# Performance work log

Measured on AMD Instinct MI355X. Metric: run time of the kernel, lower is better.

The kernel has to match this reference:

```python
import jax, jax.numpy as jnp
import numpy as np

EPS = 1e-5

def splice(x, offsets):
    # x: [B, F, T]; offsets already shifted so offsets[0] == 0.
    # Output channel order matches torch reshape(-1, C*F): y[b, f*C+c, t] = x[b, f, t+off[c]]
    w = offsets[-1]
    Tn = x.shape[2] - w
    y = jnp.stack([x[:, :, o:o + Tn] for o in offsets], axis=2)  # [B, F, C, Tn]
    B, F, C, _ = y.shape
    return y.reshape(B, F * C, Tn)

def conv1x1(x, w, b):
    # x: [B, Cin, T], w: [Cout, Cin], b: [Cout]
    return jnp.einsum('oc,bct->bot', w, x) + b[None, :, None]

def bn_ct(x, gamma=None, beta=None):
    # BatchNorm1d (training mode, biased var) over (batch, time) per channel
    m = x.mean(axis=(0, 2), keepdims=True)
    v = x.var(axis=(0, 2), keepdims=True)
    y = (x - m) * jax.lax.rsqrt(v + EPS)
    if gamma is not None:
        y = y * gamma[None, :, None] + beta[None, :, None]
    return y

def bn_c(x, gamma, beta):
    # BatchNorm1d on [B, C]
    m = x.mean(axis=0, keepdims=True)
    v = x.var(axis=0, keepdims=True)
    return (x - m) * jax.lax.rsqrt(v + EPS) * gamma[None, :] + beta[None, :]

def relu6(x):
    return jnp.clip(x, 0.0, 6.0)

def setup_inputs() -> dict:
    key = jax.random.key(0)
    ks = list(jax.random.split(key, 32))
    def rn(shape, scale=0.05):
        return jax.random.normal(ks.pop(), shape, dtype=jnp.float32) * scale
    inp = {
        'x': jax.random.normal(ks.pop(), (32, 2048, 20), dtype=jnp.float32),
        'h1_w': rn((512, 100)), 'h1_b': rn((512,)),
        'h2_w': rn((512, 1536)), 'h2_b': rn((512,)),
        'bn2_g': jnp.ones((512,), jnp.float32), 'bn2_b': jnp.zeros((512,), jnp.float32),
        'h3_w': rn((512, 1536)), 'h3_b': rn((512,)),
        'bn3_g': jnp.ones((512,), jnp.float32), 'bn3_b': jnp.zeros((512,), jnp.float32),
        'h4_w': rn((512, 512)), 'h4_b': rn((512,)),
        'bn4_g': jnp.ones((512,), jnp.float32), 'bn4_b': jnp.zeros((512,), jnp.float32),
        'h5_w': rn((1500, 512)), 'h5_b': rn((1500,)),
        'bn5_g': jnp.ones((1500,), jnp.float32), 'bn5_b': jnp.zeros((1500,), jnp.float32),
        'l1_w': rn((512, 3000)), 'l1_b': rn((512,)),
        'bn6_g': jnp.ones((512,), jnp.float32), 'bn6_b': jnp.zeros((512,), jnp.float32),
        'l2_w': rn((512, 512)), 'l2_b': rn((512,)),
        'bn7_g': jnp.ones((512,), jnp.float32), 'bn7_b': jnp.zeros((512,), jnp.float32),
    }
    return inp

def reference(x, h1_w, h1_b, h2_w, h2_b, bn2_g, bn2_b, h3_w, h3_b, bn3_g, bn3_b,
              h4_w, h4_b, bn4_g, bn4_b, h5_w, h5_b, bn5_g, bn5_b,
              l1_w, l1_b, bn6_g, bn6_b, l2_w, l2_b, bn7_g, bn7_b):
    o = jnp.transpose(x, (0, 2, 1))                     # [B, 20, T]
    o = splice(o, (0, 1, 2, 3, 4))                      # context [-2..2] -> [B, 100, T-4]
    o = bn_ct(jax.nn.relu(conv1x1(o, h1_w, h1_b)))      # bn1 affine=False
    o = splice(o, (0, 2, 4))                            # context [-2,0,2] -> [B, 1536, T-8]
    o = bn_ct(jax.nn.relu(conv1x1(o, h2_w, h2_b)), bn2_g, bn2_b)
    o = splice(o, (0, 3, 6))                            # context [-3,0,3] -> [B, 1536, T-14]
    o = bn_ct(jax.nn.relu(conv1x1(o, h3_w, h3_b)), bn3_g, bn3_b)
    o = bn_ct(relu6(conv1x1(o, h4_w, h4_b)), bn4_g, bn4_b)
    o = bn_ct(relu6(conv1x1(o, h5_w, h5_b)), bn5_g, bn5_b)  # [B, 1500, T']
    mean = o.mean(axis=-1)
    std = jnp.std(o, axis=-1, ddof=1)                   # torch.std is unbiased
    o = jnp.concatenate((mean, std), axis=1)            # [B, 3000]
    o = bn_c(relu6(o @ l1_w.T + l1_b), bn6_g, bn6_b)
    o = bn_c(relu6(o @ l2_w.T + l2_b), bn7_g, bn7_b)
    return o
```

## Files before the change

### kernel.cpp

```cpp
#include <hip/hip_runtime.h>
#include <cstdint>

#define EPSF 1e-5f

namespace {

typedef _Float16 f16;
typedef _Float16 v8h __attribute__((ext_vector_type(8)));
typedef float v4f __attribute__((ext_vector_type(4)));

constexpr int B  = 32;
constexpr int T0 = 2048, F0 = 20;
constexpr int T1 = 2044, T2 = 2040, T3 = 2034;
constexpr int TS = 2048;

__device__ __forceinline__ void gload16(const void* g, void* l) {
    typedef const __attribute__((address_space(1))) void* gp_t;
    typedef __attribute__((address_space(3))) void* lp_t;
    __builtin_amdgcn_global_load_lds((gp_t)(unsigned long long)g,
                                     (lp_t)(unsigned int)(unsigned long long)l,
                                     16, 0, 0);
}
__device__ __forceinline__ void wait_vm6() { asm volatile("s_waitcnt vmcnt(6)" ::: "memory"); }
__device__ __forceinline__ void wait_vm4() { asm volatile("s_waitcnt vmcnt(4)" ::: "memory"); }
__device__ __forceinline__ void wait_vm0() { asm volatile("s_waitcnt vmcnt(0)" ::: "memory"); }

#define BARRIER asm volatile("s_barrier" ::: "memory")

__global__ __launch_bounds__(256) void transpose_x(const float* __restrict__ x,
                                                   f16* __restrict__ xT,
                                                   float* __restrict__ stZ)
{
    int idx = blockIdx.x * 256 + threadIdx.x;
    if (idx < 4096) stZ[idx] = 0.f;
    constexpr int total = B * 3 * TS * 8;
    if (idx >= total) return;
    int fl = idx & 7;
    int t  = (idx >> 3) & (TS - 1);
    int fo = (idx >> 14) % 3;
    int b  = idx / (3 << 14);
    int f  = fo * 8 + fl;
    float v = (f < F0) ? x[((size_t)b * T0 + t) * F0 + f] : 0.f;
    xT[idx] = (f16)v;
}

template<int FP, int C>
__global__ __launch_bounds__(256) void fold_mfma(
    const float* __restrict__ W, const float* __restrict__ bias,
    const float* __restrict__ st, const float* __restrict__ gamma, const float* __restrict__ beta,
    f16* __restrict__ Wh, float* __restrict__ bf,
    int Oreal, int Freal, int Cin, int CinOrig, float invN)
{
    int o = blockIdx.x;
    auto sidx = [&](int k) {
        return ((size_t)((o >> 7) * (Cin >> 3) + (k >> 3)) * 128 + (o & 127)) * 8 + (k & 7);
    };
    if (o >= Oreal) {
        for (int k = threadIdx.x; k < Cin; k += 256) Wh[sidx(k)] = (f16)0.f;
        if (threadIdx.x == 0) bf[o] = 0.f;
        return;
    }
    float local = 0.f;
    for (int k = threadIdx.x; k < Cin; k += 256) {
        int c = k / FP, f = k - c * FP;
        float wv = 0.f;
        if (c < C && f < Freal) {
            float sc = 1.f, sh = 0.f;
            if (st) {
                float mean = st[f] * invN;
                float var  = st[Freal + f] * invN - mean * mean;
                sc = rsqrtf(var + EPSF);
                if (gamma) sc *= gamma[f];
                sh = (beta ? beta[f] : 0.f) - mean * sc;
            }
            float w = W[(size_t)o * CinOrig + f * C + c];
            wv = w * sc;
            local += w * sh;
        }
        Wh[sidx(k)] = (f16)wv;
    }
#pragma unroll
    for (int d = 32; d; d >>= 1) local += __shfl_down(local, d);
    __shared__ float red[4];
    if ((threadIdx.x & 63) == 0) red[threadIdx.x >> 6] = local;
    __syncthreads();
    if (threadIdx.x == 0) bf[o] = bias[o] + red[0] + red[1] + red[2] + red[3];
}

template<int ACT, int FPR, int CIN>
__global__ __launch_bounds__(256, 4) void conv_mfma(
    const f16* __restrict__ inT, const f16* __restrict__ Wh,
    const float* __restrict__ bias, f16* __restrict__ outT,
    float* __restrict__ st, int O, int Tout, int offMul)
{
    __shared__ __align__(16) f16 Ilds[2][4 * 128 * 8];
    __shared__ __align__(16) f16 Wlds[2][4 * 128 * 8];
    __shared__ float redS[2][128];
    __shared__ float redQ[2][128];
    const int tid  = threadIdx.x;
    const int lane = tid & 63, wave = tid >> 6;
    const int wt = wave & 1, wo = wave >> 1;
    const int quad = lane >> 4, l16 = lane & 15;
    const int tB = blockIdx.x * 128, oB = blockIdx.y * 128, b = blockIdx.z;
    const f16* inb = inT + (size_t)b * FPR * TS;
    const size_t wBase = (size_t)(oB >> 7) * (CIN >> 3);

    v4f acc[4][4];
#pragma unroll
    for (int mi = 0; mi < 4; ++mi)
#pragma unroll
        for (int ni = 0; ni < 4; ++ni)
#pragma unroll
            for (int r = 0; r < 4; ++r) acc[mi][ni][r] = 0.f;

    constexpr int nIter = CIN >> 5;

    auto compute = [&](int pb) {
        v8h afr[4], bfr[4];
#pragma unroll
        for (int mi = 0; mi < 4; ++mi)
            afr[mi] = *(const v8h*)&Ilds[pb][(quad * 128 + wt * 64 + mi * 16 + l16) * 8];
#pragma unroll
        for (int ni = 0; ni < 4; ++ni)
            bfr[ni] = *(const v8h*)&Wlds[pb][(quad * 128 + wo * 64 + ni * 16 + l16) * 8];
#pragma unroll
        for (int mi = 0; mi < 4; ++mi)
#pragma unroll
            for (int ni = 0; ni < 4; ++ni)
                acc[mi][ni] = __builtin_amdgcn_mfma_f32_16x16x32_f16(
                    afr[mi], bfr[ni], acc[mi][ni], 0, 0, 0);
    };

    auto stage = [&](int iB, int pb) {
#pragma unroll
        for (int j = 0; j < 4; ++j) {
            int s = wave * 4 + j;
            int koct = (s & 7) >> 1, half = s & 1;
            if (s < 8) {
                int kidx = iB + koct * 8;
                int c = kidx / FPR, f = kidx - c * FPR;
                int t = tB + half * 64 + lane + c * offMul;
                gload16(inb + ((size_t)(f >> 3) * TS + t) * 8,
                        &Ilds[pb][(koct * 128 + half * 64) * 8]);
            } else {
                gload16(Wh + ((wBase + (iB >> 3) + koct) * 128 + half * 64 + lane) * 8,
                        &Wlds[pb][(koct * 128 + half * 64) * 8]);
            }
        }
    };
    stage(0, 0);
#pragma unroll 2
    for (int k = 0; k < nIter; ++k) {
        const int pb = k & 1;
        __syncthreads();
        if (k + 1 < nIter) { stage((k + 1) * 32, pb ^ 1); wait_vm4(); }
        else               { wait_vm0(); }
        __syncthreads();
        compute(pb);
    }

    float Sl[4] = {0, 0, 0, 0}, Ql[4] = {0, 0, 0, 0};
#pragma unroll
    for (int ni = 0; ni < 4; ++ni) {
        const int o  = oB + wo * 64 + ni * 16 + l16;
        const float bs = bias[o];
        f16* orow = outT + (size_t)b * O * TS + (size_t)(o >> 3) * TS * 8 + (o & 7);
#pragma unroll
        for (int mi = 0; mi < 4; ++mi)
#pragma unroll
            for (int r = 0; r < 4; ++r) {
                int t = tB + wt * 64 + mi * 16 + quad * 4 + r;
                if (t < Tout) {
                    float v = acc[mi][ni][r] + bs;
                    v = fmaxf(v, 0.f);
                    if (ACT == 2) v = fminf(v, 6.f);
                    orow[(size_t)t * 8] = (f16)v;
                    Sl[ni] += v; Ql[ni] += v * v;
                }
            }
    }
#pragma unroll
    for (int ni = 0; ni < 4; ++ni) {
        float s = Sl[ni], q = Ql[ni];
        s += __shfl_down(s, 32); q += __shfl_down(q, 32);
        s += __shfl_down(s, 16); q += __shfl_down(q, 16);
        if (lane < 16) {
            redS[wt][wo * 64 + ni * 16 + lane] = s;
            redQ[wt][wo * 64 + ni * 16 + lane] = q;
        }
    }
    __syncthreads();
    if (tid < 128) {
        atomicAdd(&st[oB + tid],       redS[0][tid] + redS[1][tid]);
        atomicAdd(&st[512 + oB + tid], redQ[0][tid] + redQ[1][tid]);
    }
}


#define LDSB_M(PB, NH) do {                                                          \
    _Pragma("unroll")                                                                \
    for (int n2 = 0; n2 < 2; ++n2) {                                                 \
        _Pragma("unroll")                                                            \
        for (int ks = 0; ks < 2; ++ks)                                               \
            bfr[NH][n2][ks] = *(const v8h*)&Wlds[PB][((ks * 4 + quad) * 256 +        \
                (NH) * 128 + wo * 32 + n2 * 16 + l16) * 8];                          \
    }                                                                                \
} while (0)

#define MFMA_Q(MH, NH) do {                                                          \
    asm volatile("s_waitcnt lgkmcnt(0)" ::: "memory");                               \
    __builtin_amdgcn_sched_barrier(0);                                               \
    __builtin_amdgcn_s_setprio(1);                                                   \
    _Pragma("unroll")                                                                \
    for (int m4 = 0; m4 < 4; ++m4) {                                                 \
        _Pragma("unroll")                                                            \
        for (int n2 = 0; n2 < 2; ++n2) {                                             \
            _Pragma("unroll")                                                        \
            for (int ks = 0; ks < 2; ++ks)                                           \
                acc[(MH) * 4 + m4][(NH) * 2 + n2] =                                  \
                    __builtin_amdgcn_mfma_f32_16x16x32_f16(                          \
                        afr[m4][ks], bfr[NH][n2][ks],                                \
                        acc[(MH) * 4 + m4][(NH) * 2 + n2], 0, 0, 0);                 \
        }                                                                            \
    }                                                                                \
    __builtin_amdgcn_s_setprio(0);                                                   \
} while (0)

template<int ACT, int CIN, bool POOL>
__global__ __launch_bounds__(512, 2) void conv8p(
    const f16* __restrict__ inT, const f16* __restrict__ Wh,
    const float* __restrict__ bias, f16* __restrict__ outT,
    float* __restrict__ st, float* __restrict__ Sp, float* __restrict__ Qp,
    int O, int Tout, int offMul, int Opad)
{
    constexpr bool SPLICE = (CIN == 1536);
    constexpr int NT = CIN / 64;
    constexpr int nIter = NT / 2;
    __shared__ __align__(16) f16 Ilds[2][8 * 256 * 8];
    __shared__ __align__(16) f16 Wlds[2][8 * 256 * 8];
    __shared__ float redS[8][64];
    __shared__ float redQ[8][64];

    const int tid = threadIdx.x;
    const int lane = tid & 63, wave = tid >> 6;
    const int wt = wave & 1, wo = wave >> 1;
    const int quad = lane >> 4, l16 = lane & 15;
    const int tB = blockIdx.x * 256, oB = blockIdx.y * 256, b = blockIdx.z;
    const f16* inb = inT + (size_t)b * 64 * TS * 8;
    const int sBase = oB >> 7;
    const int octSel = tid >> 7;
    const int tPos = tid & 127;

    auto stageA = [&](int pb, int kt, int mh) {
#pragma unroll
        for (int cc = 0; cc < 2; ++cc) {
            const int octL = cc * 4 + octSel;
            const int octG = kt * 8 + octL;
            const int t = tB + mh * 128 + tPos;
            const f16* src;
            if constexpr (SPLICE) {
                const int cx = octG >> 6;
                const int fo = octG & 63;
                src = inb + ((size_t)fo * TS + t + cx * offMul) * 8;
            } else {
                src = inb + ((size_t)octG * TS + t) * 8;
            }
            gload16(src, &Ilds[pb][(octL * 256 + mh * 128 + tPos) * 8]);
        }
    };
    auto stageB = [&](int pb, int kt, int nh) {
#pragma unroll
        for (int cc = 0; cc < 2; ++cc) {
            const int octL = cc * 4 + octSel;
            const f16* src = Wh + (((size_t)(sBase + nh) * (CIN >> 3) + kt * 8 + octL) * 128 + tPos) * 8;
            gload16(src, &Wlds[pb][(octL * 256 + nh * 128 + tPos) * 8]);
        }
    };

    v4f acc[8][4];
#pragma unroll
    for (int m = 0; m < 8; ++m)
#pragma unroll
        for (int n = 0; n < 4; ++n)
#pragma unroll
            for (int r = 0; r < 4; ++r) acc[m][n][r] = 0.f;

    v8h afr[4][2];
    v8h bfr[2][2][2];

    auto ldsA = [&](int pb, int mh) {
#pragma unroll
        for (int m4 = 0; m4 < 4; ++m4)
#pragma unroll
            for (int ks = 0; ks < 2; ++ks)
                afr[m4][ks] = *(const v8h*)&Ilds[pb][((ks * 4 + quad) * 256 +
                    mh * 128 + wt * 64 + m4 * 16 + l16) * 8];
    };

    stageA(0, 0, 0); stageB(0, 0, 0);
    stageB(0, 0, 1); stageA(0, 0, 1);
    stageA(1, 1, 0); stageB(1, 1, 0); stageB(1, 1, 1);
    wait_vm6();
    BARRIER;

#pragma unroll 1
    for (int i = 0; i < nIter; ++i) {
        const int kt1 = 2 * i + 1;
        const int kn0 = 2 * i + 2, kn1 = 2 * i + 3;
        const bool more = (i + 1 < nIter);
        ldsA(0, 0); LDSB_M(0, 0);
        stageA(1, kt1, 1);
        BARRIER;
        MFMA_Q(0, 0);
        BARRIER;
        LDSB_M(0, 1);
        if (more) stageA(0, kn0, 0);
        BARRIER;
        MFMA_Q(0, 1);
        BARRIER;
        ldsA(0, 1);
        if (more) stageB(0, kn0, 0);
        BARRIER;
        MFMA_Q(1, 0);
        BARRIER;
        if (more) { stageB(0, kn0, 1); wait_vm6(); } else wait_vm0();
        BARRIER;
        MFMA_Q(1, 1);
        BARRIER;
        ldsA(1, 0); LDSB_M(1, 0);
        if (more) stageA(0, kn0, 1);
        BARRIER;
        MFMA_Q(0, 0);
        BARRIER;
        LDSB_M(1, 1);
        if (more) stageA(1, kn1, 0);
        BARRIER;
        MFMA_Q(0, 1);
        BARRIER;
        ldsA(1, 1);
        if (more) stageB(1, kn1, 0);
        BARRIER;
        MFMA_Q(1, 0);
        BARRIER;
        if (more) { stageB(1, kn1, 1); wait_vm6(); }
        BARRIER;
        MFMA_Q(1, 1);
        BARRIER;
    }

    float Sl[4] = {0, 0, 0, 0}, Ql[4] = {0, 0, 0, 0};
#pragma unroll
    for (int n = 0; n < 4; ++n) {
        const int oLoc = (n >> 1) * 128 + wo * 32 + (n & 1) * 16 + l16;
        const int o = oB + oLoc;
        const float bs = bias[o];
        f16* orow = nullptr;
        if constexpr (!POOL)
            orow = outT + (size_t)b * O * TS + (size_t)(o >> 3) * TS * 8 + (o & 7);
#pragma unroll
        for (int m = 0; m < 8; ++m)
#pragma unroll
            for (int r = 0; r < 4; ++r) {
                const int t = tB + (m >> 2) * 128 + wt * 64 + (m & 3) * 16 + quad * 4 + r;
                if (t < Tout) {
                    float v = acc[m][n][r] + bs;
                    v = fmaxf(v, 0.f);
                    if (ACT == 2) v = fminf(v, 6.f);
                    if constexpr (!POOL) orow[(size_t)t * 8] = (f16)v;
                    Sl[n] += v; Ql[n] += v * v;
                }
            }
    }
#pragma unroll
    for (int n = 0; n < 4; ++n) {
        float s = Sl[n], q = Ql[n];
        s += __shfl_down(s, 32); q += __shfl_down(q, 32);
        s += __shfl_down(s, 16); q += __shfl_down(q, 16);
        if (lane < 16) { redS[wave][n * 16 + lane] = s; redQ[wave][n * 16 + lane] = q; }
    }
    __syncthreads();
    if (tid < 256) {
        const int rem = tid & 127;
        const int wo2 = rem >> 5;
        const int nn  = (tid >> 7) * 2 + ((rem >> 4) & 1);
        const int l   = tid & 15;
        const float s = redS[wo2 * 2][nn * 16 + l] + redS[wo2 * 2 + 1][nn * 16 + l];
        const float q = redQ[wo2 * 2][nn * 16 + l] + redQ[wo2 * 2 + 1][nn * 16 + l];
        if constexpr (POOL) {
            Sp[((size_t)blockIdx.x * B + b) * Opad + oB + tid] = s;
            Qp[((size_t)blockIdx.x * B + b) * Opad + oB + tid] = q;
        } else {
            atomicAdd(&st[oB + tid], s);
            atomicAdd(&st[512 + oB + tid], q);
        }
    }
}

__global__ __launch_bounds__(256) void pool_finalize(
    const float* __restrict__ Sp, const float* __restrict__ Qp,
    const float* __restrict__ g5, const float* __restrict__ b5,
    float* __restrict__ stat, int Opad, int Oreal, int T)
{
    int co = blockIdx.x * 256 + threadIdx.x;
    if (co >= Oreal) return;
    double sS = 0, sQ = 0;
    for (int z = 0; z < 8; ++z)
        for (int b = 0; b < B; ++b) {
            sS += Sp[((size_t)z * B + b) * Opad + co];
            sQ += Qp[((size_t)z * B + b) * Opad + co];
        }
    double invN = 1.0 / ((double)B * T);
    double m = sS * invN;
    double v = sQ * invN - m * m;
    float sc = g5[co] * rsqrtf((float)v + EPSF);
    float sh = b5[co] - (float)m * sc;
    for (int b = 0; b < B; ++b) {
        double sb = 0, qb = 0;
        for (int z = 0; z < 8; ++z) {
            sb += Sp[((size_t)z * B + b) * Opad + co];
            qb += Qp[((size_t)z * B + b) * Opad + co];
        }
        double mb = sb / T;
        double vb = (qb - sb * sb / T) / (T - 1);
        if (vb < 0) vb = 0;
        stat[(size_t)b * 2 * Oreal + co]         = (float)mb * sc + sh;
        stat[(size_t)b * 2 * Oreal + Oreal + co] = sqrtf((float)vb) * fabsf(sc);
    }
}

__global__ __launch_bounds__(256) void fc_relu6(const float* __restrict__ x,
                                                const float* __restrict__ W,
                                                const float* __restrict__ bias,
                                                float* __restrict__ y, int Cin, int O)
{
    int wid = (blockIdx.x * 256 + threadIdx.x) >> 6;
    int lane = threadIdx.x & 63;
    if (wid >= B * O) return;
    int b = wid / O, o = wid - b * O;
    const float* xr = x + (size_t)b * Cin;
    const float* wr = W + (size_t)o * Cin;
    float s = 0.f;
    for (int c = lane; c < Cin; c += 64) s = fmaf(xr[c], wr[c], s);
#pragma unroll
    for (int d = 32; d; d >>= 1) s += __shfl_down(s, d);
    if (lane == 0) y[wid] = fminf(fmaxf(s + bias[o], 0.f), 6.f);
}

__global__ __launch_bounds__(512) void bn_batch(const float* __restrict__ x,
                                                const float* __restrict__ g,
                                                const float* __restrict__ be,
                                                float* __restrict__ y, int O)
{
    int o = threadIdx.x;
    if (o >= O) return;
    float s = 0.f, q = 0.f;
    for (int b = 0; b < B; ++b) { float v = x[b * O + o]; s += v; q += v * v; }
    float m = s / B;
    float var = q / B - m * m;
    float sc = g[o] * rsqrtf(var + EPSF);
    float sh = be[o] - m * sc;
    for (int b = 0; b < B; ++b) y[b * O + o] = x[b * O + o] * sc + sh;
}

}

extern "C" void kernel_launch(void* const* d_in, const int* in_sizes, int n_in,
                              void* d_out, int out_size, void* d_ws, size_t ws_size,
                              hipStream_t stream)
{
    (void)in_sizes; (void)n_in; (void)out_size; (void)ws_size;
    const float* x     = (const float*)d_in[0];
    const float* h1_w  = (const float*)d_in[1];
    const float* h1_b  = (const float*)d_in[2];
    const float* h2_w  = (const float*)d_in[3];
    const float* h2_b  = (const float*)d_in[4];
    const float* bn2_g = (const float*)d_in[5];
    const float* bn2_b = (const float*)d_in[6];
    const float* h3_w  = (const float*)d_in[7];
    const float* h3_b  = (const float*)d_in[8];
    const float* bn3_g = (const float*)d_in[9];
    const float* bn3_b = (const float*)d_in[10];
    const float* h4_w  = (const float*)d_in[11];
    const float* h4_b  = (const float*)d_in[12];
    const float* bn4_g = (const float*)d_in[13];
    const float* bn4_b = (const float*)d_in[14];
    const float* h5_w  = (const float*)d_in[15];
    const float* h5_b  = (const float*)d_in[16];
    const float* bn5_g = (const float*)d_in[17];
    const float* bn5_b = (const float*)d_in[18];
    const float* l1_w  = (const float*)d_in[19];
    const float* l1_b  = (const float*)d_in[20];
    const float* bn6_g = (const float*)d_in[21];
    const float* bn6_b = (const float*)d_in[22];
    const float* l2_w  = (const float*)d_in[23];
    const float* l2_b  = (const float*)d_in[24];
    const float* bn7_g = (const float*)d_in[25];
    const float* bn7_b = (const float*)d_in[26];

    char* ws = (char*)d_ws;
    size_t off = 0;
    auto alloc = [&](size_t bytes) {
        char* p = ws + off;
        off += (bytes + 255) & ~(size_t)255;
        return (void*)p;
    };
    f16* xT    = (f16*)alloc(((size_t)B * 3  * TS * 8 + 2048) * 2);
    f16* bufA  = (f16*)alloc(((size_t)B * 64 * TS * 8 + 2048) * 2);
    f16* bufB  = (f16*)alloc(((size_t)B * 64 * TS * 8 + 2048) * 2);
    f16* Wh1   = (f16*)alloc((size_t)512 * 128 * 2);
    f16* Wh2   = (f16*)alloc((size_t)512 * 1536 * 2);
    f16* Wh3   = (f16*)alloc((size_t)512 * 1536 * 2);
    f16* Wh4   = (f16*)alloc((size_t)512 * 512 * 2);
    f16* Wh5   = (f16*)alloc((size_t)1536 * 512 * 2);
    float* bf1 = (float*)alloc(512 * 4);
    float* bf2 = (float*)alloc(512 * 4);
    float* bf3 = (float*)alloc(512 * 4);
    float* bf4 = (float*)alloc(512 * 4);
    float* bf5 = (float*)alloc(1536 * 4);
    float* stZ = (float*)alloc(4096 * 4);
    float* st1 = stZ, *st2 = stZ + 1024, *st3 = stZ + 2048, *st4 = stZ + 3072;
    float* Sp  = (float*)alloc((size_t)8 * B * 1536 * 4);
    float* Qp  = (float*)alloc((size_t)8 * B * 1536 * 4);
    float* stat = (float*)alloc((size_t)B * 3000 * 4);
    float* f1  = (float*)alloc((size_t)B * 512 * 4);
    float* f2  = (float*)alloc((size_t)B * 512 * 4);

    transpose_x<<<(B * 3 * TS * 8 + 255) / 256, 256, 0, stream>>>(x, xT, stZ);

    fold_mfma<24, 5><<<512, 256, 0, stream>>>(h1_w, h1_b, nullptr, nullptr, nullptr,
                                              Wh1, bf1, 512, 20, 128, 100, 0.f);
    conv_mfma<1, 24, 128><<<dim3(16, 4, B), 256, 0, stream>>>(
        xT, Wh1, bf1, bufA, st1, 512, T1, 1);

    fold_mfma<512, 3><<<512, 256, 0, stream>>>(h2_w, h2_b, st1, nullptr, nullptr,
                                               Wh2, bf2, 512, 512, 1536, 1536,
                                               1.f / (B * T1));
    conv8p<1, 1536, false><<<dim3(8, 2, B), 512, 0, stream>>>(
        bufA, Wh2, bf2, bufB, st2, nullptr, nullptr, 512, T2, 2, 0);

    fold_mfma<512, 3><<<512, 256, 0, stream>>>(h3_w, h3_b, st2, bn2_g, bn2_b,
                                               Wh3, bf3, 512, 512, 1536, 1536,
                                               1.f / (B * T2));
    conv8p<1, 1536, false><<<dim3(8, 2, B), 512, 0, stream>>>(
        bufB, Wh3, bf3, bufA, st3, nullptr, nullptr, 512, T3, 3, 0);

    fold_mfma<512, 1><<<512, 256, 0, stream>>>(h4_w, h4_b, st3, bn3_g, bn3_b,
                                               Wh4, bf4, 512, 512, 512, 512,
                                               1.f / (B * T3));
    conv8p<2, 512, false><<<dim3(8, 2, B), 512, 0, stream>>>(
        bufA, Wh4, bf4, bufB, st4, nullptr, nullptr, 512, T3, 0, 0);

    fold_mfma<512, 1><<<1536, 256, 0, stream>>>(h5_w, h5_b, st4, bn4_g, bn4_b,
                                                Wh5, bf5, 1500, 512, 512, 512,
                                                1.f / (B * T3));
    conv8p<2, 512, true><<<dim3(8, 6, B), 512, 0, stream>>>(
        bufB, Wh5, bf5, nullptr, nullptr, Sp, Qp, 1536, T3, 0, 1536);

    pool_finalize<<<6, 256, 0, stream>>>(Sp, Qp, bn5_g, bn5_b, stat, 1536, 1500, T3);

    fc_relu6<<<(B * 512 * 64 + 255) / 256, 256, 0, stream>>>(stat, l1_w, l1_b, f1, 3000, 512);
    bn_batch<<<1, 512, 0, stream>>>(f1, bn6_g, bn6_b, f1, 512);
    fc_relu6<<<(B * 512 * 64 + 255) / 256, 256, 0, stream>>>(f1, l2_w, l2_b, f2, 512, 512);
    bn_batch<<<1, 512, 0, stream>>>(f2, bn7_g, bn7_b, (float*)d_out, 512);
}
```

Baseline: 676.4 us.

## Double-buffer A fragments and use partial lgkmcnt waits in conv8p main loop

The conv GEMM main loop now keeps two register sets of A fragments and issues LDS reads for the next quadrant before the current MFMA block. Each MFMA block waits only for the LDS reads it needs (partial lgkmcnt) instead of all of them. The global-to-LDS staging order and vmcnt thresholds are rearranged to match, so LDS read latency overlaps with matrix math. The cost is more VGPRs under a 512-thread, 2-block launch bound, and the hand-counted wait values are fragile.

```diff
diff --git a/kernel.cpp b/kernel.cpp
--- a/kernel.cpp
+++ b/kernel.cpp
@@ -21,7 +21,7 @@
                                      (lp_t)(unsigned int)(unsigned long long)l,
                                      16, 0, 0);
 }
-__device__ __forceinline__ void wait_vm6() { asm volatile("s_waitcnt vmcnt(6)" ::: "memory"); }
+__device__ __forceinline__ void wait_vm8() { asm volatile("s_waitcnt vmcnt(8)" ::: "memory"); }
 __device__ __forceinline__ void wait_vm4() { asm volatile("s_waitcnt vmcnt(4)" ::: "memory"); }
 __device__ __forceinline__ void wait_vm0() { asm volatile("s_waitcnt vmcnt(0)" ::: "memory"); }
 
@@ -197,18 +197,8 @@
 }
 
 
-#define LDSB_M(PB, NH) do {                                                          \
-    _Pragma("unroll")                                                                \
-    for (int n2 = 0; n2 < 2; ++n2) {                                                 \
-        _Pragma("unroll")                                                            \
-        for (int ks = 0; ks < 2; ++ks)                                               \
-            bfr[NH][n2][ks] = *(const v8h*)&Wlds[PB][((ks * 4 + quad) * 256 +        \
-                (NH) * 128 + wo * 32 + n2 * 16 + l16) * 8];                          \
-    }                                                                                \
-} while (0)
-
-#define MFMA_Q(MH, NH) do {                                                          \
-    asm volatile("s_waitcnt lgkmcnt(0)" ::: "memory");                               \
+#define MQ(MH, NH, G, LGSTR) do {                                                    \
+    asm volatile("s_waitcnt lgkmcnt(" LGSTR ")" ::: "memory");                       \
     __builtin_amdgcn_sched_barrier(0);                                               \
     __builtin_amdgcn_s_setprio(1);                                                   \
     _Pragma("unroll")                                                                \
@@ -219,7 +209,7 @@
             for (int ks = 0; ks < 2; ++ks)                                           \
                 acc[(MH) * 4 + m4][(NH) * 2 + n2] =                                  \
                     __builtin_amdgcn_mfma_f32_16x16x32_f16(                          \
-                        afr[m4][ks], bfr[NH][n2][ks],                                \
+                        aS[G][m4][ks], bS[NH][n2][ks],                               \
                         acc[(MH) * 4 + m4][(NH) * 2 + n2], 0, 0, 0);                 \
         }                                                                            \
     }                                                                                \
@@ -285,67 +275,63 @@
 #pragma unroll
             for (int r = 0; r < 4; ++r) acc[m][n][r] = 0.f;
 
-    v8h afr[4][2];
-    v8h bfr[2][2][2];
-
-    auto ldsA = [&](int pb, int mh) {
+    v8h aS[2][4][2];
+    v8h bS[2][2][2];
+
+    auto rdA = [&](int pb, int mh, int g) {
 #pragma unroll
         for (int m4 = 0; m4 < 4; ++m4)
 #pragma unroll
             for (int ks = 0; ks < 2; ++ks)
-                afr[m4][ks] = *(const v8h*)&Ilds[pb][((ks * 4 + quad) * 256 +
+                aS[g][m4][ks] = *(const v8h*)&Ilds[pb][((ks * 4 + quad) * 256 +
                     mh * 128 + wt * 64 + m4 * 16 + l16) * 8];
     };
-
-    stageA(0, 0, 0); stageB(0, 0, 0);
-    stageB(0, 0, 1); stageA(0, 0, 1);
-    stageA(1, 1, 0); stageB(1, 1, 0); stageB(1, 1, 1);
-    wait_vm6();
+    auto rdB = [&](int pb, int nh) {
+#pragma unroll
+        for (int n2 = 0; n2 < 2; ++n2)
+#pragma unroll
+            for (int ks = 0; ks < 2; ++ks)
+                bS[nh][n2][ks] = *(const v8h*)&Wlds[pb][((ks * 4 + quad) * 256 +
+                    nh * 128 + wo * 32 + n2 * 16 + l16) * 8];
+    };
+
+    stageA(0, 0, 0); stageB(0, 0, 0); stageB(0, 0, 1); stageA(0, 0, 1);
+    stageA(1, 1, 0); stageB(1, 1, 0); stageB(1, 1, 1); stageA(1, 1, 1);
+    wait_vm8();
     BARRIER;
+    rdA(0, 0, 0); rdB(0, 0);
 
 #pragma unroll 1
     for (int i = 0; i < nIter; ++i) {
-        const int kt1 = 2 * i + 1;
         const int kn0 = 2 * i + 2, kn1 = 2 * i + 3;
         const bool more = (i + 1 < nIter);
-        ldsA(0, 0); LDSB_M(0, 0);
-        stageA(1, kt1, 1);
+        rdB(0, 1);
+        BARRIER; MQ(0, 0, 0, "4"); BARRIER;
+        rdA(0, 1, 1);
+        if (more) stageA(0, kn0, 0);
+        BARRIER; MQ(0, 1, 0, "8"); BARRIER;
+        if (more) stageB(0, kn0, 0);
+        BARRIER; MQ(1, 0, 1, "0");
+        if (more) wait_vm4(); else wait_vm0();
         BARRIER;
-        MFMA_Q(0, 0);
+        rdA(1, 0, 0); rdB(1, 0);
+        if (more) stageB(0, kn0, 1);
+        BARRIER; MQ(1, 1, 1, "12"); BARRIER;
+        rdB(1, 1);
+        if (more) stageA(0, kn0, 1);
+        BARRIER; MQ(0, 0, 0, "4"); BARRIER;
+        rdA(1, 1, 1);
+        if (more) stageA(1, kn1, 0);
+        BARRIER; MQ(0, 1, 0, "8"); BARRIER;
+        if (more) stageB(1, kn1, 0);
+        BARRIER; MQ(1, 0, 1, "0");
+        if (more) wait_vm4();
         BARRIER;
-        LDSB_M(0, 1);
-        if (more) stageA(0, kn0, 0);
-        BARRIER;
-        MFMA_Q(0, 1);
-        BARRIER;
-        ldsA(0, 1);
-        if (more) stageB(0, kn0, 0);
-        BARRIER;
-        MFMA_Q(1, 0);
-        BARRIER;
-        if (more) { stageB(0, kn0, 1); wait_vm6(); } else wait_vm0();
-        BARRIER;
-        MFMA_Q(1, 1);
-        BARRIER;
-        ldsA(1, 0); LDSB_M(1, 0);
-        if (more) stageA(0, kn0, 1);
-        BARRIER;
-        MFMA_Q(0, 0);
-        BARRIER;
-        LDSB_M(1, 1);
-        if (more) stageA(1, kn1, 0);
-        BARRIER;
-        MFMA_Q(0, 1);
-        BARRIER;
-        ldsA(1, 1);
-        if (more) stageB(1, kn1, 0);
-        BARRIER;
-        MFMA_Q(1, 0);
-        BARRIER;
-        if (more) { stageB(1, kn1, 1); wait_vm6(); }
-        BARRIER;
-        MFMA_Q(1, 1);
-        BARRIER;
+        if (more) {
+            rdA(0, 0, 0); rdB(0, 0);
+            stageB(1, kn1, 1); stageA(1, kn1, 1);
+        }
+        BARRIER; MQ(1, 1, 1, "12"); BARRIER;
     }
 
     float Sl[4] = {0, 0, 0, 0}, Ql[4] = {0, 0, 0, 0};
```

Result: slower. 868.6 us (+28.4%).
